# Performance work log

Measured on AMD Instinct MI355X. Metric: run time of the kernel, lower is better.

Reference implementation:

```python
import jax, jax.numpy as jnp
import numpy as np
import math

C = 128
A_SCALES = [2.0, 4.0, 8.0]
A_RATIOS = [0.5, 1.0, 2.0]
STRIDES = [4, 8, 16, 32, 64]
NA = len(A_SCALES) * len(A_RATIOS)
IMG = 1024
N = 2
NMS_THRESH = 0.7
NUM_PRE = 6000
NUM_POST = 300
SCALE_CLIP = math.log(1000.0 / 16.0)


def base_anchors(stride):
    c = stride / 2.0
    a = []
    for s in A_SCALES:
        for r in A_RATIOS:
            h = stride * s * math.sqrt(r)
            w = stride * s * math.sqrt(1.0 / r)
            a.append((c - h / 2.0, c - w / 2.0, c + h / 2.0, c + w / 2.0))
    return np.array(a, dtype=np.float32)  # [NA,4] yxyx


def shifted_anchors(stride, H, W):
    base = jnp.asarray(base_anchors(stride))
    gy = jnp.arange(H, dtype=jnp.float32) * stride
    gx = jnp.arange(W, dtype=jnp.float32) * stride
    grid = jnp.stack(jnp.meshgrid(gy, gx, indexing='ij'), axis=-1)  # [H,W,2]
    shift = jnp.concatenate([grid, grid], axis=-1)  # [H,W,4]
    return (base[None, None] + shift[:, :, None]).reshape(-1, 4)  # [H*W*NA,4]


def conv(x, w, b, pad):
    y = jax.lax.conv_general_dilated(x, w, (1, 1), pad, dimension_numbers=('NCHW', 'OIHW', 'NCHW'))
    return y + b[None, :, None, None]


def head(x, w1, b1, wobj, bobj, wbbx, bbbx):
    h = jax.nn.relu(conv(x, w1, b1, 'SAME'))
    obj = conv(h, wobj, bobj, 'VALID')  # [N,NA,H,W]
    bbx = conv(h, wbbx, bbbx, 'VALID')  # [N,4*NA,H,W]
    n = x.shape[0]
    obj = obj.transpose(0, 2, 3, 1).reshape(n, -1)       # (h,w,anchor) order
    bbx = bbx.transpose(0, 2, 3, 1).reshape(n, -1, 4)
    return obj, bbx


def shift_boxes(anchors, deltas):
    yx = (anchors[..., :2] + anchors[..., 2:]) * 0.5
    hw = anchors[..., 2:] - anchors[..., :2]
    yx_o = yx + deltas[..., :2] * hw
    hw_o = hw * jnp.exp(jnp.minimum(deltas[..., 2:], SCALE_CLIP))
    return jnp.concatenate([yx_o - 0.5 * hw_o, yx_o + 0.5 * hw_o], axis=-1)


def nms_single(boxes, scores):
    # greedy hard NMS; boxes [P,4] yxyx, scores [P]; fixed NUM_POST outputs
    areas = (boxes[:, 2] - boxes[:, 0]) * (boxes[:, 3] - boxes[:, 1])

    def step(active, _):
        masked = jnp.where(active, scores, -jnp.inf)
        i = jnp.argmax(masked)
        ok = active[i]
        tl = jnp.maximum(boxes[i, :2], boxes[:, :2])
        br = jnp.minimum(boxes[i, 2:], boxes[:, 2:])
        inter = jnp.clip(br[:, 0] - tl[:, 0], 0.0) * jnp.clip(br[:, 1] - tl[:, 1], 0.0)
        iou = inter / (areas[i] + areas - inter + 1e-9)
        active = active & (iou <= NMS_THRESH)
        return active, (jnp.where(ok, i, 0), ok)

    _, (idx, valid) = jax.lax.scan(step, jnp.ones(boxes.shape[0], bool), None, length=NUM_POST)
    return idx, valid


def forward(x0, x1, x2, x3, x4, w1, b1, wobj, bobj, wbbx, bbbx, valid_size):
    feats = [x0, x1, x2, x3, x4]
    objs, bbxs, ancs = [], [], []
    for f, s in zip(feats, STRIDES):
        o, b = head(f, w1, b1, wobj, bobj, wbbx, bbbx)
        objs.append(o)
        bbxs.append(b)
        ancs.append(shifted_anchors(s, f.shape[2], f.shape[3]))
    obj = jnp.concatenate(objs, axis=1)        # [N,M]
    bbx = jnp.concatenate(bbxs, axis=1)        # [N,M,4]
    anchors = jnp.concatenate(ancs, axis=0)    # [M,4]
    boxes = shift_boxes(anchors[None], bbx)    # [N,M,4]
    h = valid_size[:, 0].astype(boxes.dtype)[:, None]
    w = valid_size[:, 1].astype(boxes.dtype)[:, None]
    boxes = jnp.stack([jnp.clip(boxes[..., 0], 0.0, h),
                       jnp.clip(boxes[..., 1], 0.0, w),
                       jnp.clip(boxes[..., 2], 0.0, h),
                       jnp.clip(boxes[..., 3], 0.0, w)], axis=-1)
    k = min(boxes.shape[1], NUM_PRE)
    top_scores, top_idx = jax.lax.top_k(obj, k)                     # per-image topk
    top_boxes = jnp.take_along_axis(boxes, top_idx[..., None], axis=1)
    idx, valid = jax.vmap(nms_single)(jax.lax.stop_gradient(top_boxes),
                                      jax.lax.stop_gradient(top_scores))
    props = jnp.take_along_axis(top_boxes, idx[..., None], axis=1)  # [N,NUM_POST,4]
    props = props * valid[..., None].astype(props.dtype)            # zero-pad invalid
    return props, valid


def setup_inputs() -> dict:
    key = jax.random.key(0)
    ks = jax.random.split(key, 8)
    sizes = [IMG // s for s in STRIDES]
    inp = {}
    for i, hw in enumerate(sizes):
        inp['x%d' % i] = jax.random.normal(ks[i], (N, C, hw, hw), jnp.float32)
    inp['w1'] = jax.random.normal(ks[5], (C, C, 3, 3), jnp.float32) * 0.05
    inp['b1'] = jnp.zeros((C,), jnp.float32)
    inp['wobj'] = jax.random.normal(ks[6], (NA, C, 1, 1), jnp.float32) * 0.05
    inp['bobj'] = jnp.zeros((NA,), jnp.float32)
    inp['wbbx'] = jax.random.normal(ks[7], (4 * NA, C, 1, 1), jnp.float32) * 0.05
    inp['bbbx'] = jnp.zeros((4 * NA,), jnp.float32)
    inp['valid_size'] = jnp.array([[IMG, IMG]] * N, jnp.int32)
    return inp


def reference(x0, x1, x2, x3, x4, w1, b1, wobj, bobj, wbbx, bbbx, valid_size):
    return forward(x0, x1, x2, x3, x4, w1, b1, wobj, bobj, wbbx, bbbx, valid_size)
```

## Files before the change

### kernel.cpp

```cpp
#include <hip/hip_runtime.h>
#include <stdint.h>
#include <math.h>

#define M_TOT 785664
#define NPRE  6000
#define NPOST 300
#define CAP   8192
#define NWORDS 94
#define ROWW   96
#define NPAD   6016

__device__ __forceinline__ uint32_t okey(float f) {
    uint32_t u = __float_as_uint(f);
    return (u & 0x80000000u) ? ~u : (u | 0x80000000u);
}

__global__ void k_zero(uint32_t* p, int n) {
    int i = blockIdx.x * blockDim.x + threadIdx.x;
    if (i < n) p[i] = 0u;
}

__global__ void k_wt(const float* __restrict__ w1, float* __restrict__ wt) {
    int i = blockIdx.x * 256 + threadIdx.x;
    if (i >= 128 * 128 * 9) return;
    int co = i / 1152; int r = i % 1152; int ci = r / 9; int tap = r % 9;
    wt[ci * 1152 + tap * 128 + co] = w1[i];
}

__global__ __launch_bounds__(512) void k_conv(
    const float* __restrict__ x0, const float* __restrict__ x1,
    const float* __restrict__ x2, const float* __restrict__ x3,
    const float* __restrict__ x4,
    const float* __restrict__ wt, const float* __restrict__ b1,
    const float* __restrict__ wobj, const float* __restrict__ bobj,
    const float* __restrict__ wbbx, const float* __restrict__ bbbx,
    float* __restrict__ sc, float* __restrict__ dl)
{
    __shared__ __attribute__((aligned(16))) float sx[8][18][20];
    __shared__ __attribute__((aligned(16))) float sw[8 * 9 * 128];

    int b = blockIdx.x, L = 0;
    if (b >= 512) { b -= 512; L = 1;
        if (b >= 128) { b -= 128; L = 2;
            if (b >= 32) { b -= 32; L = 3;
                if (b >= 8) { b -= 8; L = 4; } } } }
    const float* xs = (L == 0) ? x0 : (L == 1) ? x1 : (L == 2) ? x2 : (L == 3) ? x3 : x4;
    const int scoff_[5] = {0, 589824, 737280, 774144, 783360};
    int Wl = 256 >> L; int Hl = Wl; int HW = Wl * Wl;
    int tpiSh = 8 - 2 * L;
    int n  = b >> tpiSh;
    int r  = b & ((1 << tpiSh) - 1);
    int txSh = 4 - L;
    int ty0 = r >> txSh, tx0 = r & ((1 << txSh) - 1);
    int y0 = ty0 << 4, x0c = tx0 << 4;
    const float* xin = xs + (size_t)n * 128 * HW;

    int t = threadIdx.x;
    int tx = t & 15;
    int ty = t >> 4;
    int py = ty >> 1, px = (ty & 1) << 3;

    float acc0[4][8], acc1[4][8];
#pragma unroll
    for (int c = 0; c < 4; ++c)
#pragma unroll
        for (int e = 0; e < 8; ++e) { acc0[c][e] = 0.f; acc1[c][e] = 0.f; }

    for (int cc0 = 0; cc0 < 128; cc0 += 8) {
        __syncthreads();
        for (int i = t; i < 2880; i += 512) {
            int ci = i / 360; int rm = i % 360; int rr = rm / 20; int cc = rm % 20;
            float v = 0.f;
            int gy = y0 - 1 + rr, gx = x0c - 1 + cc;
            if (cc < 18 && gy >= 0 && gy < Hl && gx >= 0 && gx < Wl)
                v = xin[(size_t)(cc0 + ci) * HW + (size_t)gy * Wl + gx];
            sx[ci][rr][cc] = v;
        }
        {
            const float4* wsrc = (const float4*)(wt + (size_t)cc0 * 1152);
            float4* wdst = (float4*)sw;
            for (int i = t; i < 2304; i += 512) wdst[i] = wsrc[i];
        }
        __syncthreads();

#pragma unroll 1
        for (int ci = 0; ci < 8; ++ci) {
#pragma unroll
            for (int dy = 0; dy < 3; ++dy) {
                const float* xr = &sx[ci][py + dy][px];
                float4 xa = *(const float4*)(xr);
                float4 xb = *(const float4*)(xr + 4);
                float4 xc = *(const float4*)(xr + 8);
                float win[12] = {xa.x, xa.y, xa.z, xa.w, xb.x, xb.y, xb.z, xb.w,
                                 xc.x, xc.y, xc.z, xc.w};
#pragma unroll
                for (int dx = 0; dx < 3; ++dx) {
                    const float* wr = &sw[(ci * 9 + dy * 3 + dx) * 128 + tx * 4];
                    float4 wa = *(const float4*)(wr);
                    float4 wb = *(const float4*)(wr + 64);
                    float wva[4] = {wa.x, wa.y, wa.z, wa.w};
                    float wvb[4] = {wb.x, wb.y, wb.z, wb.w};
#pragma unroll
                    for (int e = 0; e < 8; ++e) {
                        float xv = win[e + dx];
#pragma unroll
                        for (int c = 0; c < 4; ++c) {
                            acc0[c][e] = fmaf(wva[c], xv, acc0[c][e]);
                            acc1[c][e] = fmaf(wvb[c], xv, acc1[c][e]);
                        }
                    }
                }
            }
        }
    }

#pragma unroll
    for (int c = 0; c < 4; ++c) {
        float ba = b1[tx * 4 + c];
        float bb = b1[64 + tx * 4 + c];
#pragma unroll
        for (int e = 0; e < 8; ++e) {
            float v0 = acc0[c][e] + ba;
            float v1 = acc1[c][e] + bb;
            acc0[c][e] = v0 > 0.f ? v0 : 0.f;
            acc1[c][e] = v1 > 0.f ? v1 : 0.f;
        }
    }

    int gy = y0 + py;
    size_t ppos = (size_t)gy * Wl + x0c + px;
    size_t scbase = (size_t)n * M_TOT + scoff_[L];
    size_t dlbase = (size_t)n * 4 * (size_t)M_TOT + 4 * (size_t)scoff_[L];
    for (int a = 0; a < 45; ++a) {
        const float* wp = (a < 9) ? (wobj + (size_t)a * 128) : (wbbx + (size_t)(a - 9) * 128);
        float4 wa = *(const float4*)(wp + tx * 4);
        float4 wb = *(const float4*)(wp + 64 + tx * 4);
        float wva[4] = {wa.x, wa.y, wa.z, wa.w};
        float wvb[4] = {wb.x, wb.y, wb.z, wb.w};
        float p[8];
#pragma unroll
        for (int e = 0; e < 8; ++e) p[e] = 0.f;
#pragma unroll
        for (int c = 0; c < 4; ++c)
#pragma unroll
            for (int e = 0; e < 8; ++e) {
                p[e] = fmaf(wva[c], acc0[c][e], p[e]);
                p[e] = fmaf(wvb[c], acc1[c][e], p[e]);
            }
#pragma unroll
        for (int mm = 1; mm < 16; mm <<= 1)
#pragma unroll
            for (int e = 0; e < 8; ++e)
                p[e] += __shfl_xor(p[e], mm, 64);
        if (tx == 0) {
            float bias = (a < 9) ? bobj[a] : bbbx[a - 9];
            float4 o0 = make_float4(p[0] + bias, p[1] + bias, p[2] + bias, p[3] + bias);
            float4 o1 = make_float4(p[4] + bias, p[5] + bias, p[6] + bias, p[7] + bias);
            float* dst = (a < 9) ? (sc + scbase + (size_t)a * HW + ppos)
                                 : (dl + dlbase + (size_t)(a - 9) * HW + ppos);
            *(float4*)dst = o0;
            *(float4*)(dst + 4) = o1;
        }
    }
}

__global__ __launch_bounds__(256) void k_hist(const float* __restrict__ sc,
                                              uint32_t* __restrict__ hist) {
    __shared__ uint32_t lh[8192];
    int n = blockIdx.y;
    for (int i = threadIdx.x; i < 8192; i += 256) lh[i] = 0u;
    __syncthreads();
    const float* s = sc + (size_t)n * M_TOT;
    int stride = gridDim.x * 256;
    for (int i = blockIdx.x * 256 + threadIdx.x; i < M_TOT; i += stride)
        atomicAdd(&lh[okey(s[i]) >> 19], 1u);
    __syncthreads();
    for (int i = threadIdx.x; i < 8192; i += 256) {
        uint32_t v = lh[i];
        if (v) atomicAdd(&hist[n * 8192 + i], v);
    }
}

__global__ void k_subhist(const float* __restrict__ sc, const uint32_t* __restrict__ ctrl,
                          uint32_t* __restrict__ subh) {
    int i = blockIdx.x * blockDim.x + threadIdx.x;
    int stride = gridDim.x * blockDim.x;
    for (; i < 2 * M_TOT; i += stride) {
        int n = i >= M_TOT;
        uint32_t k = okey(sc[i]);
        if ((k >> 19) == ctrl[n * 8 + 0])
            atomicAdd(&subh[n * 8192 + ((k >> 6) & 0x1FFFu)], 1u);
    }
}

__global__ void k_scan(const uint32_t* __restrict__ hist, uint32_t* __restrict__ ctrl, int phase) {
    int n = blockIdx.x;
    const uint32_t* h = hist + n * 8192;
    uint32_t* c = ctrl + n * 8;
    __shared__ uint32_t tp[256];
    int t = threadIdx.x;
    uint32_t s = 0;
    for (int r = 0; r < 32; ++r) s += h[8191 - (t * 32 + r)];
    tp[t] = s;
    __syncthreads();
    if (t == 0) {
        uint32_t run = (phase == 0) ? 0u : c[1];
        for (int i = 0; i < 256; ++i) { uint32_t v = tp[i]; tp[i] = run; run += v; }
    }
    __syncthreads();
    uint32_t cum = tp[t];
    for (int r = 0; r < 32; ++r) {
        int j = 8191 - (t * 32 + r);
        uint32_t cc = h[j];
        if (cum < 6000u && cum + cc >= 6000u) {
            if (phase == 0) { c[0] = (uint32_t)j; c[1] = cum; }
            else            { c[2] = (c[0] << 19) | ((uint32_t)j << 6); }
        }
        cum += cc;
    }
}

__global__ void k_compact(const float* __restrict__ sc, uint32_t* __restrict__ ctrl,
                          uint64_t* __restrict__ cand) {
    int i = blockIdx.x * blockDim.x + threadIdx.x;
    int stride = gridDim.x * blockDim.x;
    const int scoff_[5] = {0, 589824, 737280, 774144, 783360};
    int lane = threadIdx.x & 63;
    for (; i < 2 * M_TOT; i += stride) {
        int n = i >= M_TOT;
        int q = n ? (i - M_TOT) : i;
        uint32_t k = okey(sc[i]);
        bool hit = (k >= ctrl[n * 8 + 2]);
        unsigned long long m = __ballot(hit);
        if (m) {
            int leader = __builtin_ctzll(m);
            uint32_t base = 0;
            if (lane == leader) base = atomicAdd(&ctrl[n * 8 + 3], (uint32_t)__popcll(m));
            base = (uint32_t)__shfl((int)base, leader, 64);
            if (hit) {
                uint32_t slot = base + (uint32_t)__popcll(m & ((1ull << lane) - 1ull));
                if (slot < CAP) {
                    int Lq = (q < 589824) ? 0 : (q < 737280) ? 1 : (q < 774144) ? 2
                            : (q < 783360) ? 3 : 4;
                    int r = q - scoff_[Lq];
                    int sh = 16 - 2 * Lq;
                    int a = r >> sh;
                    int pos = r & ((1 << sh) - 1);
                    uint32_t mm = (uint32_t)(scoff_[Lq] + pos * 9 + a);
                    cand[(size_t)n * CAP + slot] = ((uint64_t)k << 32) | (uint32_t)(~mm);
                }
            }
        }
    }
}

__global__ __launch_bounds__(256) void k_rank(const uint64_t* __restrict__ cand,
                                              const uint32_t* __restrict__ ctrl,
                                              uint64_t* __restrict__ sorted) {
    __shared__ uint64_t chunk[2048];
    int n = blockIdx.y;
    uint32_t cnt = ctrl[n * 8 + 3];
    if (cnt > CAP) cnt = CAP;
    const uint64_t* cb = cand + (size_t)n * CAP;
    uint64_t* sb = sorted + (size_t)n * CAP;
    int i = blockIdx.x * 256 + threadIdx.x;
    uint64_t key = (i < (int)cnt) ? cb[i] : 0ull;
    uint32_t rank = 0;
    for (uint32_t base = 0; base < cnt; base += 2048) {
        __syncthreads();
        for (int j = threadIdx.x; j < 2048; j += 256) {
            uint32_t idx = base + (uint32_t)j;
            chunk[j] = (idx < cnt) ? cb[idx] : 0ull;
        }
        __syncthreads();
        uint32_t lim = cnt - base; if (lim > 2048u) lim = 2048u;
        for (uint32_t j = 0; j < lim; ++j) rank += (chunk[j] > key) ? 1u : 0u;
    }
    if (i < (int)cnt && rank < CAP) sb[rank] = key;
}

__global__ void k_decode(const uint64_t* __restrict__ cand, const float* __restrict__ dl,
                         const int* __restrict__ vsz, float* __restrict__ boxes) {
    int i = blockIdx.x * 256 + threadIdx.x;
    if (i >= 2 * NPRE) return;
    int n = i / NPRE, rk = i % NPRE;
    const int scoff_[5] = {0, 589824, 737280, 774144, 783360};
    uint64_t pk = cand[(size_t)n * CAP + rk];
    uint32_t m = ~(uint32_t)(pk & 0xFFFFFFFFull);
    int Lq = (m < 589824u) ? 0 : (m < 737280u) ? 1 : (m < 774144u) ? 2 : (m < 783360u) ? 3 : 4;
    int r = (int)m - scoff_[Lq];
    int pos = r / 9;
    int a = r - pos * 9;
    int Wl = 256 >> Lq;
    int y = pos >> (8 - Lq);
    int xx = pos & (Wl - 1);
    float stridef = (float)(4 << Lq);
    double sD = (double)(2 << (a / 3));
    double rD = ((a % 3) == 0) ? 0.5 : ((a % 3) == 1) ? 1.0 : 2.0;
    double hD = ((double)stridef * sD) * sqrt(rD);
    double wD = ((double)stridef * sD) * sqrt(1.0 / rD);
    double cD = (double)stridef / 2.0;
    float y1b = (float)(cD - hD / 2.0);
    float x1b = (float)(cD - wD / 2.0);
    float y2b = (float)(cD + hD / 2.0);
    float x2b = (float)(cD + wD / 2.0);
    float gy = (float)y * stridef;
    float gx = (float)xx * stridef;
    float ay1 = __fadd_rn(y1b, gy), ax1 = __fadd_rn(x1b, gx);
    float ay2 = __fadd_rn(y2b, gy), ax2 = __fadd_rn(x2b, gx);
    float cy = __fmul_rn(__fadd_rn(ay1, ay2), 0.5f);
    float cx = __fmul_rn(__fadd_rn(ax1, ax2), 0.5f);
    float ah = __fsub_rn(ay2, ay1);
    float aw = __fsub_rn(ax2, ax1);
    size_t HWl = (size_t)Wl * Wl;
    size_t db = (size_t)n * 4 * M_TOT + 4 * (size_t)scoff_[Lq] + (size_t)pos;
    float dy_ = dl[db + (size_t)(a * 4 + 0) * HWl];
    float dx_ = dl[db + (size_t)(a * 4 + 1) * HWl];
    float dh_ = dl[db + (size_t)(a * 4 + 2) * HWl];
    float dw_ = dl[db + (size_t)(a * 4 + 3) * HWl];
    float yo = __fadd_rn(cy, __fmul_rn(dy_, ah));
    float xo = __fadd_rn(cx, __fmul_rn(dx_, aw));
    const float SCLIPf = 4.135166556742356f;
    float ho = __fmul_rn(ah, (float)exp((double)fminf(dh_, SCLIPf)));
    float wo = __fmul_rn(aw, (float)exp((double)fminf(dw_, SCLIPf)));
    float hf = (float)vsz[n * 2 + 0], wf = (float)vsz[n * 2 + 1];
    float y1 = fminf(fmaxf(__fsub_rn(yo, __fmul_rn(0.5f, ho)), 0.f), hf);
    float x1 = fminf(fmaxf(__fsub_rn(xo, __fmul_rn(0.5f, wo)), 0.f), wf);
    float y2 = fminf(fmaxf(__fadd_rn(yo, __fmul_rn(0.5f, ho)), 0.f), hf);
    float x2 = fminf(fmaxf(__fadd_rn(xo, __fmul_rn(0.5f, wo)), 0.f), wf);
    *(float4*)(boxes + ((size_t)n * NPAD + rk) * 4) = make_float4(y1, x1, y2, x2);
}

__global__ __launch_bounds__(256) void k_iou(const float* __restrict__ boxes,
                                             uint64_t* __restrict__ ioum) {
    int n = blockIdx.y;
    int i = blockIdx.x * 4 + (threadIdx.x >> 6);
    int lane = threadIdx.x & 63;
    const float* bsrc = boxes + (size_t)n * NPAD * 4;
    float4 bi = *(const float4*)(bsrc + (size_t)i * 4);
    float ai = __fmul_rn(__fsub_rn(bi.z, bi.x), __fsub_rn(bi.w, bi.y));
    uint64_t* row = ioum + ((size_t)n * NPAD + i) * ROWW;
    int w0 = i >> 6;
    for (int w = lane; w < w0; w += 64) row[w] = 0ull;
    for (int w = w0; w < NWORDS; ++w) {
        int j = (w << 6) | lane;
        bool pred = false;
        if (j > i && j < NPRE) {
            float4 bj = *(const float4*)(bsrc + (size_t)j * 4);
            float aj = __fmul_rn(__fsub_rn(bj.z, bj.x), __fsub_rn(bj.w, bj.y));
            float ty = fmaxf(bi.x, bj.x), tx2 = fmaxf(bi.y, bj.y);
            float by = fminf(bi.z, bj.z), bx2 = fminf(bi.w, bj.w);
            float ih = fmaxf(__fsub_rn(by, ty), 0.f), iw = fmaxf(__fsub_rn(bx2, tx2), 0.f);
            float inter = __fmul_rn(ih, iw);
            float den = __fadd_rn(__fsub_rn(__fadd_rn(ai, aj), inter), 1e-9f);
            float iou = __fdiv_rn(inter, den);
            pred = iou > 0.7f;
        }
        unsigned long long msk = __ballot(pred);
        if (lane == 0) row[w] = (uint64_t)msk;
    }
}

__global__ __launch_bounds__(64) void k_nms(const float* __restrict__ boxes,
                                            const uint64_t* __restrict__ ioum,
                                            float* __restrict__ out) {
    int n = blockIdx.x;
    __shared__ uint64_t sup[NWORDS];
    __shared__ int keepl[NPOST];
    int lane = threadIdx.x;
    for (int w = lane; w < NWORDS; w += 64) sup[w] = 0ull;
    __syncthreads();
    int kept = 0;
    bool stop = false;
    for (int w = 0; w < NWORDS && kept < NPOST && !stop; ++w) {
        uint64_t vmask = (w == NWORDS - 1) ? ((1ull << 48) - 1ull) : ~0ull;
        uint64_t avail = (~sup[w]) & vmask;
        while (avail && kept < NPOST) {
            int bpos = __builtin_ctzll(avail);
            int i = (w << 6) | bpos;
            if (lane == 0) keepl[kept] = i;
            kept++;
            float4 bi = *(const float4*)(boxes + ((size_t)n * NPAD + i) * 4);
            float area = __fmul_rn(__fsub_rn(bi.z, bi.x), __fsub_rn(bi.w, bi.y));
            float selfiou = __fdiv_rn(area, __fadd_rn(area, 1e-9f));
            if (!(selfiou > 0.7f)) {
                if (lane == 0) { for (int k2 = kept; k2 < NPOST; ++k2) keepl[k2] = i; }
                kept = NPOST;
                stop = true;
                break;
            }
            const uint64_t* row = ioum + ((size_t)n * NPAD + i) * ROWW;
            sup[lane] |= row[lane];
            if (lane < NWORDS - 64) sup[64 + lane] |= row[64 + lane];
            __syncthreads();
            avail = (~sup[w]) & vmask & ~((2ull << bpos) - 1ull);
        }
    }
    __syncthreads();
    for (int k = lane; k < NPOST; k += 64) {
        float4 bx = make_float4(0.f, 0.f, 0.f, 0.f);
        float vf = 0.f;
        if (k < kept) {
            int i = keepl[k];
            bx = *(const float4*)(boxes + ((size_t)n * NPAD + i) * 4);
            vf = 1.f;
        }
        *(float4*)(out + (size_t)n * 1200 + (size_t)k * 4) = bx;
        out[2400 + n * 300 + k] = vf;
    }
}

__global__ __launch_bounds__(256) void k_diag(const uint32_t* __restrict__ ctrl,
                                              const uint64_t* __restrict__ sorted,
                                              const float* __restrict__ boxes,
                                              float* __restrict__ out) {
    __shared__ unsigned sfl;
    if (threadIdx.x == 0) sfl = 0u;
    __syncthreads();
    unsigned fl = 0;
    for (int n = 0; n < 2; ++n) {
        if (threadIdx.x == 0) {
            uint32_t cnt = ctrl[n * 8 + 3];
            if (cnt < 6000u || cnt > (uint32_t)CAP) fl |= 1u << n;
        }
        for (int r = threadIdx.x + 1; r < NPRE; r += 256)
            if (sorted[(size_t)n * CAP + r - 1] <= sorted[(size_t)n * CAP + r])
                fl |= 4u << n;
        for (int r = threadIdx.x; r < NPRE * 4; r += 256) {
            float v = boxes[(size_t)n * NPAD * 4 + r];
            if (!(v >= 0.0f && v <= 1024.0f)) fl |= 16u << n;
        }
    }
    if (fl) atomicOr(&sfl, fl);
    __syncthreads();
    if (threadIdx.x == 0 && sfl) out[0] = 65536.0f * (float)(1u + sfl);
}

extern "C" void kernel_launch(void* const* d_in, const int* in_sizes, int n_in,
                              void* d_out, int out_size, void* d_ws, size_t ws_size,
                              hipStream_t stream) {
    (void)out_size; (void)ws_size;
    static const int want[12] = {16777216, 4194304, 1048576, 262144, 65536,
                                 147456, 128, 1152, 9, 4608, 36, 4};
    const void* p[12];
    for (int k = 0; k < 12; ++k) p[k] = d_in[k];
    bool pos_ok = (n_in >= 12);
    for (int k = 0; k < 12 && pos_ok; ++k) if (in_sizes[k] != want[k]) pos_ok = false;
    if (!pos_ok) {
        for (int k = 0; k < 12; ++k)
            for (int j = 0; j < n_in; ++j)
                if (in_sizes[j] == want[k]) { p[k] = d_in[j]; break; }
    }
    const float* x0   = (const float*)p[0];
    const float* x1   = (const float*)p[1];
    const float* x2   = (const float*)p[2];
    const float* x3   = (const float*)p[3];
    const float* x4   = (const float*)p[4];
    const float* w1   = (const float*)p[5];
    const float* b1   = (const float*)p[6];
    const float* wobj = (const float*)p[7];
    const float* bobj = (const float*)p[8];
    const float* wbbx = (const float*)p[9];
    const float* bbbx = (const float*)p[10];
    const int*   vsz  = (const int*)p[11];
    float* out = (float*)d_out;

    size_t off = 0;
    char* base = (char*)d_ws;
    auto carve = [&](size_t bytes) -> void* {
        void* q = base + off;
        off += (bytes + 255) & ~(size_t)255;
        return q;
    };
    float*    SC     = (float*)carve((size_t)2 * M_TOT * 4);
    float*    DL     = (float*)carve((size_t)2 * M_TOT * 16);
    float*    WT     = (float*)carve((size_t)147456 * 4);
    uint32_t* HIST   = (uint32_t*)carve((size_t)16384 * 4);
    uint32_t* SUBH   = (uint32_t*)carve((size_t)16384 * 4);
    uint32_t* CTRL   = (uint32_t*)carve((size_t)64 * 4);
    uint64_t* CAND   = (uint64_t*)carve((size_t)2 * CAP * 8);
    uint64_t* SORTED = (uint64_t*)carve((size_t)2 * CAP * 8);
    float*    BOXES  = (float*)carve((size_t)2 * NPAD * 16);
    uint64_t* IOUM   = (uint64_t*)carve((size_t)2 * NPAD * ROWW * 8);

    int zn = (int)(((char*)CAND - (char*)HIST) / 4);
    k_zero<<<(zn + 255) / 256, 256, 0, stream>>>(HIST, zn);
    k_wt<<<(147456 + 255) / 256, 256, 0, stream>>>(w1, WT);
    k_conv<<<682, 512, 0, stream>>>(x0, x1, x2, x3, x4, WT, b1,
                                    wobj, bobj, wbbx, bbbx, SC, DL);
    k_hist<<<dim3(256, 2), 256, 0, stream>>>(SC, HIST);
    k_scan<<<2, 256, 0, stream>>>(HIST, CTRL, 0);
    k_subhist<<<1024, 256, 0, stream>>>(SC, CTRL, SUBH);
    k_scan<<<2, 256, 0, stream>>>(SUBH, CTRL, 1);
    k_compact<<<1024, 256, 0, stream>>>(SC, CTRL, CAND);
    k_rank<<<dim3(CAP / 256, 2), 256, 0, stream>>>(CAND, CTRL, SORTED);
    k_decode<<<(2 * NPRE + 255) / 256, 256, 0, stream>>>(SORTED, DL, vsz, BOXES);
    k_iou<<<dim3(NPRE / 4, 2), 256, 0, stream>>>(BOXES, IOUM);
    k_nms<<<2, 64, 0, stream>>>(BOXES, IOUM, out);
    k_diag<<<1, 256, 0, stream>>>(CTRL, SORTED, BOXES, out);
}
```

Measured before the change: 1.095 ms.

## Prefetch conv input into registers and load weights directly to LDS; precompute NMS degenerate mask

```diff
diff --git a/kernel.cpp b/kernel.cpp
--- a/kernel.cpp
+++ b/kernel.cpp
@@ -13,6 +13,13 @@
 __device__ __forceinline__ uint32_t okey(float f) {
     uint32_t u = __float_as_uint(f);
     return (u & 0x80000000u) ? ~u : (u | 0x80000000u);
+}
+
+__device__ __forceinline__ void gload_lds16(const float* g, float* l) {
+    __builtin_amdgcn_global_load_lds(
+        (__attribute__((address_space(1))) void*)g,
+        (__attribute__((address_space(3))) void*)l,
+        16, 0, 0);
 }
 
 __global__ void k_zero(uint32_t* p, int n) {
@@ -60,28 +67,51 @@
     int ty = t >> 4;
     int py = ty >> 1, px = (ty & 1) << 3;
 
-    float acc0[4][8], acc1[4][8];
-#pragma unroll
-    for (int c = 0; c < 4; ++c)
-#pragma unroll
-        for (int e = 0; e < 8; ++e) { acc0[c][e] = 0.f; acc1[c][e] = 0.f; }
-
-    for (int cc0 = 0; cc0 < 128; cc0 += 8) {
-        __syncthreads();
-        for (int i = t; i < 2880; i += 512) {
+    uint32_t soff[6];
+    float xvv[6];
+#pragma unroll
+    for (int k = 0; k < 6; ++k) {
+        int i = t + (k << 9);
+        uint32_t off = 0xFFFFFFFFu;
+        if (i < 2880) {
             int ci = i / 360; int rm = i % 360; int rr = rm / 20; int cc = rm % 20;
-            float v = 0.f;
             int gy = y0 - 1 + rr, gx = x0c - 1 + cc;
             if (cc < 18 && gy >= 0 && gy < Hl && gx >= 0 && gx < Wl)
-                v = xin[(size_t)(cc0 + ci) * HW + (size_t)gy * Wl + gx];
-            sx[ci][rr][cc] = v;
-        }
-        {
-            const float4* wsrc = (const float4*)(wt + (size_t)cc0 * 1152);
-            float4* wdst = (float4*)sw;
-            for (int i = t; i < 2304; i += 512) wdst[i] = wsrc[i];
-        }
-        __syncthreads();
+                off = (uint32_t)(ci * HW + gy * Wl + gx);
+        }
+        soff[k] = off;
+    }
+    float* sxf = (float*)sx;
+    float* swf = (float*)sw;
+
+    float acc0[4][8], acc1[4][8];
+#pragma unroll
+    for (int c = 0; c < 4; ++c)
+#pragma unroll
+        for (int e = 0; e < 8; ++e) { acc0[c][e] = 0.f; acc1[c][e] = 0.f; }
+
+#pragma unroll
+    for (int k = 0; k < 6; ++k)
+        xvv[k] = (soff[k] != 0xFFFFFFFFu) ? xin[soff[k]] : 0.f;
+    {
+        const float* wsrc = wt;
+#pragma unroll
+        for (int k = 0; k < 5; ++k) {
+            int i = t + (k << 9);
+            if (i < 2304) gload_lds16(wsrc + 4 * i, swf + 4 * i);
+        }
+    }
+#pragma unroll
+    for (int k = 0; k < 6; ++k) { int i = t + (k << 9); if (i < 2880) sxf[i] = xvv[k]; }
+    __syncthreads();
+
+    for (int s = 0; s < 16; ++s) {
+        if (s < 15) {
+            size_t xb = (size_t)(s + 1) * 8 * HW;
+#pragma unroll
+            for (int k = 0; k < 6; ++k)
+                xvv[k] = (soff[k] != 0xFFFFFFFFu) ? xin[xb + soff[k]] : 0.f;
+        }
 
 #pragma unroll 1
         for (int ci = 0; ci < 8; ++ci) {
@@ -111,6 +141,21 @@
                     }
                 }
             }
+        }
+
+        if (s < 15) {
+            __syncthreads();
+            {
+                const float* wsrc = wt + (size_t)(s + 1) * 8 * 1152;
+#pragma unroll
+                for (int k = 0; k < 5; ++k) {
+                    int i = t + (k << 9);
+                    if (i < 2304) gload_lds16(wsrc + 4 * i, swf + 4 * i);
+                }
+            }
+#pragma unroll
+            for (int k = 0; k < 6; ++k) { int i = t + (k << 9); if (i < 2880) sxf[i] = xvv[k]; }
+            __syncthreads();
         }
     }
 
@@ -280,7 +325,8 @@
 }
 
 __global__ void k_decode(const uint64_t* __restrict__ cand, const float* __restrict__ dl,
-                         const int* __restrict__ vsz, float* __restrict__ boxes) {
+                         const int* __restrict__ vsz, float* __restrict__ boxes,
+                         unsigned long long* __restrict__ degm) {
     int i = blockIdx.x * 256 + threadIdx.x;
     if (i >= 2 * NPRE) return;
     int n = i / NPRE, rk = i % NPRE;
@@ -329,6 +375,10 @@
     float y2 = fminf(fmaxf(__fadd_rn(yo, __fmul_rn(0.5f, ho)), 0.f), hf);
     float x2 = fminf(fmaxf(__fadd_rn(xo, __fmul_rn(0.5f, wo)), 0.f), wf);
     *(float4*)(boxes + ((size_t)n * NPAD + rk) * 4) = make_float4(y1, x1, y2, x2);
+    float area = __fmul_rn(__fsub_rn(y2, y1), __fsub_rn(x2, x1));
+    float selfiou = __fdiv_rn(area, __fadd_rn(area, 1e-9f));
+    if (!(selfiou > 0.7f))
+        atomicOr(&degm[(size_t)n * ROWW + (rk >> 6)], 1ull << (rk & 63));
 }
 
 __global__ __launch_bounds__(256) void k_iou(const float* __restrict__ boxes,
@@ -363,12 +413,17 @@
 
 __global__ __launch_bounds__(64) void k_nms(const float* __restrict__ boxes,
                                             const uint64_t* __restrict__ ioum,
+                                            const unsigned long long* __restrict__ degm,
                                             float* __restrict__ out) {
     int n = blockIdx.x;
     __shared__ uint64_t sup[NWORDS];
+    __shared__ uint64_t deg[NWORDS];
     __shared__ int keepl[NPOST];
     int lane = threadIdx.x;
-    for (int w = lane; w < NWORDS; w += 64) sup[w] = 0ull;
+    for (int w = lane; w < NWORDS; w += 64) {
+        sup[w] = 0ull;
+        deg[w] = degm[(size_t)n * ROWW + w];
+    }
     __syncthreads();
     int kept = 0;
     bool stop = false;
@@ -378,20 +433,19 @@
         while (avail && kept < NPOST) {
             int bpos = __builtin_ctzll(avail);
             int i = (w << 6) | bpos;
+            const uint64_t* row = ioum + ((size_t)n * NPAD + i) * ROWW;
+            uint64_t r0 = row[lane];
+            uint64_t r1 = (lane < NWORDS - 64) ? row[64 + lane] : 0ull;
             if (lane == 0) keepl[kept] = i;
             kept++;
-            float4 bi = *(const float4*)(boxes + ((size_t)n * NPAD + i) * 4);
-            float area = __fmul_rn(__fsub_rn(bi.z, bi.x), __fsub_rn(bi.w, bi.y));
-            float selfiou = __fdiv_rn(area, __fadd_rn(area, 1e-9f));
-            if (!(selfiou > 0.7f)) {
+            if ((deg[w] >> bpos) & 1ull) {
                 if (lane == 0) { for (int k2 = kept; k2 < NPOST; ++k2) keepl[k2] = i; }
                 kept = NPOST;
                 stop = true;
                 break;
             }
-            const uint64_t* row = ioum + ((size_t)n * NPAD + i) * ROWW;
-            sup[lane] |= row[lane];
-            if (lane < NWORDS - 64) sup[64 + lane] |= row[64 + lane];
+            sup[lane] |= r0;
+            if (lane < NWORDS - 64) sup[64 + lane] |= r1;
             __syncthreads();
             avail = (~sup[w]) & vmask & ~((2ull << bpos) - 1ull);
         }
@@ -478,6 +532,7 @@
     uint32_t* HIST   = (uint32_t*)carve((size_t)16384 * 4);
     uint32_t* SUBH   = (uint32_t*)carve((size_t)16384 * 4);
     uint32_t* CTRL   = (uint32_t*)carve((size_t)64 * 4);
+    unsigned long long* DEGM = (unsigned long long*)carve((size_t)2 * ROWW * 8);
     uint64_t* CAND   = (uint64_t*)carve((size_t)2 * CAP * 8);
     uint64_t* SORTED = (uint64_t*)carve((size_t)2 * CAP * 8);
     float*    BOXES  = (float*)carve((size_t)2 * NPAD * 16);
@@ -494,8 +549,8 @@
     k_scan<<<2, 256, 0, stream>>>(SUBH, CTRL, 1);
     k_compact<<<1024, 256, 0, stream>>>(SC, CTRL, CAND);
     k_rank<<<dim3(CAP / 256, 2), 256, 0, stream>>>(CAND, CTRL, SORTED);
-    k_decode<<<(2 * NPRE + 255) / 256, 256, 0, stream>>>(SORTED, DL, vsz, BOXES);
+    k_decode<<<(2 * NPRE + 255) / 256, 256, 0, stream>>>(SORTED, DL, vsz, BOXES, DEGM);
     k_iou<<<dim3(NPRE / 4, 2), 256, 0, stream>>>(BOXES, IOUM);
-    k_nms<<<2, 64, 0, stream>>>(BOXES, IOUM, out);
+    k_nms<<<2, 64, 0, stream>>>(BOXES, IOUM, DEGM, out);
     k_diag<<<1, 256, 0, stream>>>(CTRL, SORTED, BOXES, out);
 }
```

After: 1.072 ms. -2.1%, faster.
